# Kernel tuning notes

Measured on AMD Instinct MI355X. Metric: run time of the kernel, lower is better.

The kernel has to match this reference:

```python
import math
import jax, jax.numpy as jnp
import numpy as np

B, S, HID, NH = 8, 512, 1024, 16
D = HID // NH          # head dim = 64
SPAN = 512             # att_span = max_relative_positions = max_position_embeddings


def _linear(x, W, b):
    # torch nn.Linear: y = x @ W.T + b, W is [out, in]
    return jnp.einsum('...i,oi->...o', x, W) + b


def _heads(x):
    # [B, S, HID] -> [B, NH, S, D]
    b, s, _ = x.shape
    return x.reshape(b, s, NH, D).transpose(0, 2, 1, 3)


def setup_inputs() -> dict:
    key = jax.random.key(0)
    ks = jax.random.split(key, 16)
    f = lambda i, shape, sc=1.0: jax.random.normal(ks[i], shape, dtype=jnp.float32) * sc
    return {
        'q': f(0, (B, S, HID)),
        'k': f(1, (B, S, HID)),
        'v': f(2, (B, S, HID)),
        'attention_mask': jnp.tril(jnp.ones((S, S), dtype=bool))[None, None],  # causal [1,1,S,S]
        'Wq': f(3, (HID, HID), 0.02), 'bq': jnp.zeros((HID,), jnp.float32),
        'Wk': f(4, (HID, HID), 0.02), 'bk': jnp.zeros((HID,), jnp.float32),
        'Wv': f(5, (HID, HID), 0.02), 'bv': jnp.zeros((HID,), jnp.float32),
        'Wpk': f(6, (HID, HID), 0.02), 'bpk': jnp.zeros((HID,), jnp.float32),
        'Wpq': f(7, (HID, HID), 0.02), 'bpq': jnp.zeros((HID,), jnp.float32),
        'rel_emb': f(8, (2 * SPAN, HID), 0.02),
    }


def reference(q, k, v, attention_mask, Wq, bq, Wk, bk, Wv, bv, Wpk, bpk, Wpq, bpq, rel_emb):
    scale_factor = 3  # 1 (content) + c2p + p2c
    scale = 1.0 / math.sqrt(D * scale_factor)

    ql = _heads(_linear(q, Wq, bq))   # [B,NH,S,D]
    kl = _heads(_linear(k, Wk, bk))
    vl = _heads(_linear(v, Wv, bv))

    # content-to-content scores
    scores = jnp.einsum('bhqd,bhkd->bhqk', ql, kl) * scale

    # relative positions (no bucketing since position_buckets = -1)
    rel = jnp.arange(S)[:, None] - jnp.arange(S)[None, :]          # [S,S]
    c2p_pos = jnp.clip(rel + SPAN, 0, 2 * SPAN - 1)
    p2c_pos = jnp.clip(-rel + SPAN, 0, 2 * SPAN - 1)

    # projected relative-position embeddings -> [NH, 2*SPAN, D]
    pk = _linear(rel_emb, Wpk, bpk).reshape(2 * SPAN, NH, D).transpose(1, 0, 2)
    pq = _linear(rel_emb, Wpq, bpq).reshape(2 * SPAN, NH, D).transpose(1, 0, 2)

    # content-to-position: out[b,h,q,k] = (q . pos_key)[b,h,q, c2p_pos[q,k]]
    c2p = jnp.einsum('bhqd,hjd->bhqj', ql, pk) * scale             # [B,NH,S,2*SPAN]
    c2p = jnp.take_along_axis(c2p, jnp.broadcast_to(c2p_pos[None, None], (B, NH, S, S)), axis=-1)

    # position-to-content: gathered[b,h,k,q] = (k . pos_query)[b,h,k, p2c_pos[k,q]], then transpose
    p2c = jnp.einsum('bhkd,hjd->bhkj', kl, pq) * scale             # [B,NH,S,2*SPAN]
    p2c = jnp.take_along_axis(p2c, jnp.broadcast_to(p2c_pos[None, None], (B, NH, S, S)), axis=-1)

    scores = scores + c2p + jnp.swapaxes(p2c, -1, -2)
    # subtract detached row max (as in torch: .max(...).values.detach())
    scores = scores - jax.lax.stop_gradient(scores.max(axis=-1, keepdims=True))

    # XSoftmax: masked softmax, then zero masked positions
    neg = jnp.float32(-1e30)
    probs = jax.nn.softmax(jnp.where(attention_mask, scores, neg), axis=-1)
    probs = jnp.where(attention_mask, probs, 0.0)

    ctx = jnp.einsum('bhqk,bhkd->bhqd', probs, vl)                 # [B,NH,S,D]
    return ctx.transpose(0, 2, 1, 3).reshape(B, S, HID)
```

## Files before the change

kernel.cpp:

```cpp
#include <hip/hip_runtime.h>
#include <hip/hip_bf16.h>
#include <math.h>

#define SCALE 0.07216878364870323f
#define NEG_BIG -1e30f

typedef __attribute__((ext_vector_type(8))) short bf16x8;
typedef __attribute__((ext_vector_type(4))) short bf16x4;
typedef __attribute__((ext_vector_type(4))) float f32x4;
#define MFMA_BF16 __builtin_amdgcn_mfma_f32_16x16x32_bf16

static __device__ __forceinline__ float bf2f(__hip_bfloat16 x) { return __bfloat162float(x); }
static __device__ __forceinline__ __hip_bfloat16 f2bf(float x) { return __float2bfloat16(x); }
static __device__ __forceinline__ short f2bs(float x) {
  union { __hip_bfloat16 b; short s; } u; u.b = __float2bfloat16(x); return u.s;
}
static __device__ __forceinline__ float s2f(short v) {
  union { float f; unsigned u; } x; x.u = ((unsigned)(unsigned short)v) << 16; return x.f;
}
static __device__ __forceinline__ bf16x4 cvt4(float4 f) {
  bf16x4 r; r[0] = f2bs(f.x); r[1] = f2bs(f.y); r[2] = f2bs(f.z); r[3] = f2bs(f.w);
  return r;
}
static __device__ __forceinline__ bf16x8 ldg8(const __hip_bfloat16* p) {
  return *(const bf16x8*)p;
}
static __device__ __forceinline__ void gl_lds16(const __hip_bfloat16* g, __hip_bfloat16* l) {
  __builtin_amdgcn_global_load_lds(
      (const __attribute__((address_space(1))) void*)g,
      (__attribute__((address_space(3))) void*)l, 16, 0, 0);
}

struct CvtJob { const float* src; __hip_bfloat16* dst; int n4; };
struct CvtArgs { CvtJob j[9]; };

__global__ __launch_bounds__(256) void cvt_kernel(CvtArgs a) {
  const CvtJob jb = a.j[blockIdx.y];
  const float4* s = (const float4*)jb.src;
  bf16x4* d = (bf16x4*)jb.dst;
  const int stride = gridDim.x * 256;
  for (int i = blockIdx.x * 256 + threadIdx.x; i < jb.n4; i += stride)
    d[i] = cvt4(s[i]);
}

struct Gemm { const __hip_bfloat16* A; const __hip_bfloat16* W;
              const float* bias; __hip_bfloat16* out; int mode; int mBits; int nBlk; };
struct ProjArgs { Gemm g[5]; };

static __device__ __forceinline__ void stage256(const __hip_bfloat16* gbase,
                                                __hip_bfloat16* lbase,
                                                int wave, int lane) {
  const int r = wave * 8 + (lane >> 3);
  const int chunk = (lane & 7) ^ (lane >> 3);
#pragma unroll
  for (int c = 0; c < 4; c++) {
    gl_lds16(gbase + (size_t)(c * 64 + r) * 1024 + chunk * 8,
             lbase + (size_t)(c * 64 + wave * 8) * 64);
  }
}

__global__ __launch_bounds__(512, 2) void proj_kernel(ProjArgs pa) {
  const Gemm g = pa.g[blockIdx.y];
  if ((int)blockIdx.x >= g.nBlk) return;
  __shared__ __hip_bfloat16 As[2][256][64];
  __shared__ __hip_bfloat16 Ws[2][256][64];

  const int bid = blockIdx.x;
  const int m0 = (bid & ((1 << g.mBits) - 1)) * 256;
  const int n0 = (bid >> g.mBits) * 256;
  const int tid = threadIdx.x;
  const int wave = tid >> 6, lane = tid & 63;
  const int q16 = lane >> 4, l16 = lane & 15;
  const int wr = wave >> 2, wc = wave & 3;

  const __hip_bfloat16* Ag = g.A + (size_t)m0 * 1024;
  const __hip_bfloat16* Wg = g.W + (size_t)n0 * 1024;

  f32x4 acc[8][4] = {};

  stage256(Ag, &As[0][0][0], wave, lane);
  stage256(Wg, &Ws[0][0][0], wave, lane);

  const int l7 = l16 & 7;

  for (int t = 0; t < 16; ++t) {
    const int cur = t & 1;
    __syncthreads();
    if (t + 1 < 16) {
      const int k0n = (t + 1) * 64;
      stage256(Ag + k0n, &As[cur ^ 1][0][0], wave, lane);
      stage256(Wg + k0n, &Ws[cur ^ 1][0][0], wave, lane);
    }
    const __hip_bfloat16* Ac = &As[cur][0][0];
    const __hip_bfloat16* Wc = &Ws[cur][0][0];
#pragma unroll
    for (int ki = 0; ki < 2; ki++) {
      const int csw = ((ki * 4 + q16) ^ l7) * 8;
      bf16x8 af[8];
#pragma unroll
      for (int mi = 0; mi < 8; mi++)
        af[mi] = *(const bf16x8*)(Ac + (size_t)(wr * 128 + mi * 16 + l16) * 64 + csw);
#pragma unroll
      for (int ni = 0; ni < 4; ni++) {
        bf16x8 bw = *(const bf16x8*)(Wc + (size_t)(wc * 64 + ni * 16 + l16) * 64 + csw);
#pragma unroll
        for (int mi = 0; mi < 8; mi++)
          acc[mi][ni] = MFMA_BF16(af[mi], bw, acc[mi][ni], 0, 0, 0);
      }
    }
  }

#pragma unroll
  for (int ni = 0; ni < 4; ni++) {
    const int n = n0 + wc * 64 + ni * 16 + l16;
    const int h = n >> 6, d = n & 63;
    const float bv = g.bias[n];
#pragma unroll
    for (int mi = 0; mi < 8; mi++) {
      const int mbase = m0 + wr * 128 + mi * 16 + q16 * 4;
#pragma unroll
      for (int rr = 0; rr < 4; rr++) {
        const int m = mbase + rr;
        const float val = acc[mi][ni][rr] + bv;
        size_t oidx;
        if (g.mode == 0) {
          const int b = m >> 9, s = m & 511;
          oidx = ((size_t)((b * 16 + h) * 512 + s)) * 64 + d;
        } else if (g.mode == 1) {
          const int b = m >> 9, s = m & 511;
          oidx = ((size_t)((b * 16 + h) * 64 + d)) * 512 + s;
        } else {
          oidx = ((size_t)(h * 512 + m)) * 64 + d;
        }
        g.out[oidx] = f2bf(val);
      }
    }
  }
}

__global__ __launch_bounds__(256) void attn_kernel(
    const __hip_bfloat16* __restrict__ ql,
    const __hip_bfloat16* __restrict__ kl,
    const __hip_bfloat16* __restrict__ vlT,
    const __hip_bfloat16* __restrict__ pk,
    const __hip_bfloat16* __restrict__ pq,
    float* __restrict__ out)
{
  __shared__ float rowsum[32];
  __shared__ __align__(16) __hip_bfloat16 sc[32][520];
  __shared__ __align__(16) __hip_bfloat16 ks_[32][72];
  __shared__ __align__(16) __hip_bfloat16 pks[32][72];
  __shared__ __align__(16) __hip_bfloat16 pqs[2][32][72];
  __shared__ __hip_bfloat16 cpb[2][32][34];
  __shared__ __align__(16) __hip_bfloat16 pqbT[2][2][32][36];

  const int bid = blockIdx.x;
  const int qt = 15 - (bid >> 7);
  const int bh = bid & 127;
  const int h = bh & 15, b = bh >> 4;
  const int q0 = qt * 32;

  const __hip_bfloat16* qlp = ql + (size_t)bh * 512 * 64;
  const __hip_bfloat16* klp = kl + (size_t)bh * 512 * 64;
  const __hip_bfloat16* vtp = vlT + (size_t)bh * 64 * 512;
  const __hip_bfloat16* pkp = pk + (size_t)h * 512 * 64;
  const __hip_bfloat16* pqp = pq + (size_t)h * 512 * 64;

  const int tid = threadIdx.x, wave = tid >> 6, lane = tid & 63;
  const int q16 = lane >> 4, l16 = lane & 15;
  const int wr = wave & 1, wc = wave >> 1;

  const int rowQ = q0 + wr * 16 + l16;
  bf16x8 aq0 = ldg8(qlp + (size_t)rowQ * 64 + q16 * 8);
  bf16x8 aq1 = ldg8(qlp + (size_t)rowQ * 64 + 32 + q16 * 8);

  {
    int4 z = {0, 0, 0, 0};
    *(int4*)(&pqs[1][tid >> 3][(tid & 7) * 8]) = z;
  }

  const int kEnd = q0 + 32;
  const int nIter = kEnd >> 5;

  const int sr = tid >> 3, sseg = tid & 7;
  int4 rKv, rPKv, rPQv;
  {
    rKv  = ((const int4*)(klp + (size_t)(q0 + sr) * 64))[sseg];
    rPKv = ((const int4*)(pkp + (size_t)(0 + sr) * 64))[sseg];
    rPQv = ((const int4*)(pqp + (size_t)(0 + sr) * 64))[sseg];
  }

  f32x4 qkPrev = {};
  int k0Prev = 0, parPrev = 0;

  for (int it = 0; it < nIter; ++it) {
    const int k0 = q0 - it * 32;
    const int par = it & 1;
    __syncthreads();
    *(int4*)(&ks_[sr][sseg * 8]) = rKv;
    *(int4*)(&pks[sr][sseg * 8]) = rPKv;
    *(int4*)(&pqs[par][sr][sseg * 8]) = rPQv;
    if (it > 0) {
#pragma unroll
      for (int rr = 0; rr < 4; rr++) {
        const int qh = wr * 16 + q16 * 4 + rr;
        const int kh = wc * 16 + l16;
        if (k0Prev + kh > q0 + qh) {
          sc[qh][k0Prev + kh] = f2bf(NEG_BIG);
        } else {
          const int dlt = qh - kh;
          const float c2pv = (dlt >= 0) ? bf2f(cpb[parPrev][qh][dlt])
                                        : bf2f(cpb[parPrev ^ 1][qh][dlt + 32]);
          const float p2cv = (dlt >= 0) ? bf2f(pqbT[parPrev][1][dlt][kh])
                                        : bf2f(pqbT[parPrev][0][dlt + 32][kh]);
          float v = (qkPrev[rr] + c2pv + p2cv) * SCALE;
          v = fminf(v, 60.f); v = fmaxf(v, -60.f);
          sc[qh][k0Prev + kh] = f2bf(v);
        }
      }
    }
    __syncthreads();
    if (it + 1 < nIter) {
      const int k0n = k0 - 32, jbn = q0 - k0n;
      rKv  = ((const int4*)(klp + (size_t)(k0n + sr) * 64))[sseg];
      rPKv = ((const int4*)(pkp + (size_t)(jbn + sr) * 64))[sseg];
      rPQv = ((const int4*)(pqp + (size_t)(jbn + sr) * 64))[sseg];
    }

    const int rA = wr * 16 + l16;
    const int rB = wc * 16 + l16;
    f32x4 qk = {}, cp = {}, p0 = {}, p1 = {};
#pragma unroll
    for (int ksi = 0; ksi < 2; ksi++) {
      const int ko = ksi * 32 + q16 * 8;
      bf16x8 aq = ksi ? aq1 : aq0;
      bf16x8 ak = *(const bf16x8*)(&ks_[rA][ko]);
      bf16x8 bk = *(const bf16x8*)(&ks_[rB][ko]);
      bf16x8 bp = *(const bf16x8*)(&pks[rB][ko]);
      bf16x8 b1 = *(const bf16x8*)(&pqs[par][rB][ko]);
      bf16x8 b0 = *(const bf16x8*)(&pqs[par ^ 1][rB][ko]);
      qk = MFMA_BF16(aq, bk, qk, 0, 0, 0);
      cp = MFMA_BF16(aq, bp, cp, 0, 0, 0);
      p0 = MFMA_BF16(ak, b0, p0, 0, 0, 0);
      p1 = MFMA_BF16(ak, b1, p1, 0, 0, 0);
    }
    {
      const int cw = wc * 16 + l16;
      const int rwb = wr * 16 + q16 * 4;
      bf16x4 v0, v1;
#pragma unroll
      for (int rr = 0; rr < 4; rr++) {
        cpb[par][rwb + rr][cw] = f2bf(cp[rr]);
        v0[rr] = f2bs(p0[rr]);
        v1[rr] = f2bs(p1[rr]);
      }
      *(bf16x4*)(&pqbT[par][0][cw][rwb]) = v0;
      *(bf16x4*)(&pqbT[par][1][cw][rwb]) = v1;
    }
    qkPrev = qk; k0Prev = k0; parPrev = par;
  }
  __syncthreads();
  {
#pragma unroll
    for (int rr = 0; rr < 4; rr++) {
      const int qh = wr * 16 + q16 * 4 + rr;
      const int kh = wc * 16 + l16;
      if (k0Prev + kh > q0 + qh) {
        sc[qh][k0Prev + kh] = f2bf(NEG_BIG);
      } else {
        const int dlt = qh - kh;
        const float c2pv = (dlt >= 0) ? bf2f(cpb[parPrev][qh][dlt])
                                      : bf2f(cpb[parPrev ^ 1][qh][dlt + 32]);
        const float p2cv = (dlt >= 0) ? bf2f(pqbT[parPrev][1][dlt][kh])
                                      : bf2f(pqbT[parPrev][0][dlt + 32][kh]);
        float v = (qkPrev[rr] + c2pv + p2cv) * SCALE;
        v = fminf(v, 60.f); v = fmaxf(v, -60.f);
        sc[qh][k0Prev + kh] = f2bf(v);
      }
    }
  }
  __syncthreads();

  {
    const int row = tid >> 3, sub = tid & 7;
    float m = NEG_BIG;
    for (int c = sub * 8; c < kEnd; c += 64) {
      bf16x8 x8 = *(const bf16x8*)(&sc[row][c]);
#pragma unroll
      for (int e = 0; e < 8; e++) m = fmaxf(m, s2f(x8[e]));
    }
    for (int off = 1; off < 8; off <<= 1) m = fmaxf(m, __shfl_xor(m, off));
    float s = 0.f;
    for (int c = sub * 8; c < kEnd; c += 64) {
      bf16x8 x8 = *(const bf16x8*)(&sc[row][c]);
      bf16x8 p8;
#pragma unroll
      for (int e = 0; e < 8; e++) {
        const float p = __expf(s2f(x8[e]) - m);
        p8[e] = f2bs(p);
        s += p;
      }
      *(bf16x8*)(&sc[row][c]) = p8;
    }
    for (int off = 1; off < 8; off <<= 1) s += __shfl_xor(s, off);
    if (sub == 0) rowsum[row] = s;
  }

  f32x4 octx[2] = {};
  __hip_bfloat16 (*vt)[72] = (__hip_bfloat16 (*)[72])(&pqs[0][0][0]);
  for (int k0 = 0; k0 < kEnd; k0 += 64) {
    __syncthreads();
    {
      const int r = tid >> 2, seg = tid & 3;
      const int4* src = (const int4*)(vtp + (size_t)r * 512 + k0);
      *(int4*)(&vt[r][seg * 8])       = src[seg];
      *(int4*)(&vt[r][(seg + 4) * 8]) = src[seg + 4];
    }
    __syncthreads();
#pragma unroll
    for (int sub = 0; sub < 2; sub++) {
      const int kk = k0 + sub * 32;
      if (kk < kEnd) {
        bf16x8 af = *(const bf16x8*)(&sc[wr * 16 + l16][kk + q16 * 8]);
#pragma unroll
        for (int cs = 0; cs < 2; cs++) {
          bf16x8 bv = *(const bf16x8*)(&vt[wc * 32 + cs * 16 + l16][sub * 32 + q16 * 8]);
          octx[cs] = MFMA_BF16(af, bv, octx[cs], 0, 0, 0);
        }
      }
    }
  }

  for (int cs = 0; cs < 2; cs++) {
    const int d = wc * 32 + cs * 16 + l16;
    for (int rr = 0; rr < 4; rr++) {
      const int qh = wr * 16 + q16 * 4 + rr;
      const float val = octx[cs][rr] / rowsum[qh];
      out[((size_t)(b * 512 + q0 + qh)) * 1024 + h * 64 + d] = val;
    }
  }
}

extern "C" void kernel_launch(void* const* d_in, const int* in_sizes, int n_in,
                              void* d_out, int out_size, void* d_ws, size_t ws_size,
                              hipStream_t stream) {
  const float* q   = (const float*)d_in[0];
  const float* k   = (const float*)d_in[1];
  const float* v   = (const float*)d_in[2];
  const float* Wq  = (const float*)d_in[4];
  const float* bq  = (const float*)d_in[5];
  const float* Wk  = (const float*)d_in[6];
  const float* bk  = (const float*)d_in[7];
  const float* Wv  = (const float*)d_in[8];
  const float* bv  = (const float*)d_in[9];
  const float* Wpk = (const float*)d_in[10];
  const float* bpk = (const float*)d_in[11];
  const float* Wpq = (const float*)d_in[12];
  const float* bpq = (const float*)d_in[13];
  const float* rel = (const float*)d_in[14];
  float* out = (float*)d_out;

  char* ws = (char*)d_ws;
  const size_t MB = 1u << 20;
  __hip_bfloat16* bqi  = (__hip_bfloat16*)(ws);
  __hip_bfloat16* bki  = (__hip_bfloat16*)(ws + 8 * MB);
  __hip_bfloat16* bvi  = (__hip_bfloat16*)(ws + 16 * MB);
  __hip_bfloat16* bWq  = (__hip_bfloat16*)(ws + 24 * MB);
  __hip_bfloat16* bWk  = (__hip_bfloat16*)(ws + 26 * MB);
  __hip_bfloat16* bWv  = (__hip_bfloat16*)(ws + 28 * MB);
  __hip_bfloat16* bWpk = (__hip_bfloat16*)(ws + 30 * MB);
  __hip_bfloat16* bWpq = (__hip_bfloat16*)(ws + 32 * MB);
  __hip_bfloat16* brel = (__hip_bfloat16*)(ws + 34 * MB);
  __hip_bfloat16* wql  = (__hip_bfloat16*)(ws + 35 * MB);
  __hip_bfloat16* wkl  = (__hip_bfloat16*)(ws + 43 * MB);
  __hip_bfloat16* wvlT = (__hip_bfloat16*)(ws + 51 * MB);
  __hip_bfloat16* wpk  = (__hip_bfloat16*)(ws + 59 * MB);
  __hip_bfloat16* wpq  = (__hip_bfloat16*)(ws + 60 * MB);

  CvtArgs ca;
  ca.j[0] = { q,   bqi,  4194304 / 4 };
  ca.j[1] = { k,   bki,  4194304 / 4 };
  ca.j[2] = { v,   bvi,  4194304 / 4 };
  ca.j[3] = { Wq,  bWq,  1048576 / 4 };
  ca.j[4] = { Wk,  bWk,  1048576 / 4 };
  ca.j[5] = { Wv,  bWv,  1048576 / 4 };
  ca.j[6] = { Wpk, bWpk, 1048576 / 4 };
  ca.j[7] = { Wpq, bWpq, 1048576 / 4 };
  ca.j[8] = { rel + (size_t)512 * 1024, brel, 524288 / 4 };
  cvt_kernel<<<dim3(1024, 9), 256, 0, stream>>>(ca);

  ProjArgs pj;
  pj.g[0] = { bqi,  bWq,  bq,  wql,  0, 4, 64 };
  pj.g[1] = { bki,  bWk,  bk,  wkl,  0, 4, 64 };
  pj.g[2] = { bvi,  bWv,  bv,  wvlT, 1, 4, 64 };
  pj.g[3] = { brel, bWpk, bpk, wpk,  2, 1, 8 };
  pj.g[4] = { brel, bWpq, bpq, wpq,  2, 1, 8 };
  proj_kernel<<<dim3(64, 5), 512, 0, stream>>>(pj);

  attn_kernel<<<2048, 256, 0, stream>>>(wql, wkl, wvlT, wpk, wpq, out);
}
```

Baseline: 248.8 us.

## Interleave half-tile prefetch with MFMA phases and swap V projection operands

The projection GEMM main loop now issues its global-to-LDS prefetch in half-tile pieces spread across the four MFMA phases. It replaces __syncthreads with explicit s_barrier and vmcnt waits and raises wave priority around the MFMA bursts, so loads overlap with math instead of being issued in one block. The V projection is also computed as W·X^T (operands swapped) so the transposed output is written with contiguous stores along the sequence dimension. The hand-managed waitcnt/barrier sequencing is fragile and could race if the counts are wrong.

```diff
diff --git a/kernel.cpp b/kernel.cpp
--- a/kernel.cpp
+++ b/kernel.cpp
@@ -9,6 +9,10 @@
 typedef __attribute__((ext_vector_type(4))) short bf16x4;
 typedef __attribute__((ext_vector_type(4))) float f32x4;
 #define MFMA_BF16 __builtin_amdgcn_mfma_f32_16x16x32_bf16
+
+#define BARX()   asm volatile("s_barrier" ::: "memory")
+#define VMCNT2() asm volatile("s_waitcnt vmcnt(2)" ::: "memory")
+#define VMCNT0() asm volatile("s_waitcnt vmcnt(0)" ::: "memory")
 
 static __device__ __forceinline__ float bf2f(__hip_bfloat16 x) { return __bfloat162float(x); }
 static __device__ __forceinline__ __hip_bfloat16 f2bf(float x) { return __float2bfloat16(x); }
@@ -47,15 +51,16 @@
               const float* bias; __hip_bfloat16* out; int mode; int mBits; int nBlk; };
 struct ProjArgs { Gemm g[5]; };
 
-static __device__ __forceinline__ void stage256(const __hip_bfloat16* gbase,
-                                                __hip_bfloat16* lbase,
-                                                int wave, int lane) {
-  const int r = wave * 8 + (lane >> 3);
-  const int chunk = (lane & 7) ^ (lane >> 3);
-#pragma unroll
-  for (int c = 0; c < 4; c++) {
-    gl_lds16(gbase + (size_t)(c * 64 + r) * 1024 + chunk * 8,
-             lbase + (size_t)(c * 64 + wave * 8) * 64);
+static __device__ __forceinline__ void stage_half(const __hip_bfloat16* gtile,
+                                                  __hip_bfloat16* ltile,
+                                                  int half, int wave, int lane) {
+  const int r = lane >> 3;
+  const int chunk = (lane & 7) ^ r;
+#pragma unroll
+  for (int c = 0; c < 2; c++) {
+    const int rowbase = half * 128 + c * 64 + wave * 8;
+    gl_lds16(gtile + (size_t)(rowbase + r) * 1024 + chunk * 8,
+             ltile + (size_t)rowbase * 64);
   }
 }
 
@@ -72,64 +77,93 @@
   const int wave = tid >> 6, lane = tid & 63;
   const int q16 = lane >> 4, l16 = lane & 15;
   const int wr = wave >> 2, wc = wave & 3;
+  const int l7 = l16 & 7;
 
   const __hip_bfloat16* Ag = g.A + (size_t)m0 * 1024;
   const __hip_bfloat16* Wg = g.W + (size_t)n0 * 1024;
 
   f32x4 acc[8][4] = {};
 
-  stage256(Ag, &As[0][0][0], wave, lane);
-  stage256(Wg, &Ws[0][0][0], wave, lane);
-
-  const int l7 = l16 & 7;
+  stage_half(Ag, &As[0][0][0], 0, wave, lane);
+  stage_half(Ag, &As[0][0][0], 1, wave, lane);
+  stage_half(Wg, &Ws[0][0][0], 0, wave, lane);
+  stage_half(Wg, &Ws[0][0][0], 1, wave, lane);
+  stage_half(Ag + 64, &As[1][0][0], 0, wave, lane);
+  VMCNT2();
+  BARX();
 
   for (int t = 0; t < 16; ++t) {
     const int cur = t & 1;
-    __syncthreads();
-    if (t + 1 < 16) {
-      const int k0n = (t + 1) * 64;
-      stage256(Ag + k0n, &As[cur ^ 1][0][0], wave, lane);
-      stage256(Wg + k0n, &Ws[cur ^ 1][0][0], wave, lane);
-    }
     const __hip_bfloat16* Ac = &As[cur][0][0];
     const __hip_bfloat16* Wc = &Ws[cur][0][0];
-#pragma unroll
-    for (int ki = 0; ki < 2; ki++) {
-      const int csw = ((ki * 4 + q16) ^ l7) * 8;
-      bf16x8 af[8];
-#pragma unroll
-      for (int mi = 0; mi < 8; mi++)
-        af[mi] = *(const bf16x8*)(Ac + (size_t)(wr * 128 + mi * 16 + l16) * 64 + csw);
-#pragma unroll
-      for (int ni = 0; ni < 4; ni++) {
-        bf16x8 bw = *(const bf16x8*)(Wc + (size_t)(wc * 64 + ni * 16 + l16) * 64 + csw);
-#pragma unroll
-        for (int mi = 0; mi < 8; mi++)
-          acc[mi][ni] = MFMA_BF16(af[mi], bw, acc[mi][ni], 0, 0, 0);
-      }
-    }
+    __hip_bfloat16* An = &As[cur ^ 1][0][0];
+    __hip_bfloat16* Wn = &Ws[cur ^ 1][0][0];
+    const __hip_bfloat16* gAn = Ag + (size_t)(t + 1) * 64;
+    const __hip_bfloat16* gWn = Wg + (size_t)(t + 1) * 64;
+    const bool pf = (t + 1 < 16);
+
+#pragma unroll
+    for (int kh = 0; kh < 2; kh++) {
+      const int csw = ((kh * 4 + q16) ^ l7) * 8;
+      bf16x8 bw[4];
+#pragma unroll
+      for (int ni = 0; ni < 4; ni++)
+        bw[ni] = *(const bf16x8*)(Wc + (size_t)(wc * 64 + ni * 16 + l16) * 64 + csw);
+#pragma unroll
+      for (int mh = 0; mh < 2; mh++) {
+        bf16x8 af[4];
+#pragma unroll
+        for (int mi = 0; mi < 4; mi++)
+          af[mi] = *(const bf16x8*)(Ac + (size_t)(wr * 128 + mh * 64 + mi * 16 + l16) * 64 + csw);
+        const int ph = kh * 2 + mh;
+        if (pf) {
+          if (ph == 0)      stage_half(gAn, An, 1, wave, lane);
+          else if (ph == 1) stage_half(gWn, Wn, 0, wave, lane);
+          else if (ph == 2) stage_half(gWn, Wn, 1, wave, lane);
+        }
+        __builtin_amdgcn_s_setprio(1);
+#pragma unroll
+        for (int ni = 0; ni < 4; ni++)
+#pragma unroll
+          for (int mi = 0; mi < 4; mi++)
+            acc[mh * 4 + mi][ni] =
+                MFMA_BF16(af[mi], bw[ni], acc[mh * 4 + mi][ni], 0, 0, 0);
+        __builtin_amdgcn_s_setprio(0);
+      }
+    }
+    BARX();
+    if (t + 2 < 16) {
+      stage_half(Ag + (size_t)(t + 2) * 64, &As[cur][0][0], 0, wave, lane);
+      VMCNT2();
+    } else {
+      VMCNT0();
+    }
+    BARX();
   }
 
 #pragma unroll
   for (int ni = 0; ni < 4; ni++) {
     const int n = n0 + wc * 64 + ni * 16 + l16;
-    const int h = n >> 6, d = n & 63;
-    const float bv = g.bias[n];
 #pragma unroll
     for (int mi = 0; mi < 8; mi++) {
-      const int mbase = m0 + wr * 128 + mi * 16 + q16 * 4;
 #pragma unroll
       for (int rr = 0; rr < 4; rr++) {
-        const int m = mbase + rr;
-        const float val = acc[mi][ni][rr] + bv;
+        const int m = m0 + wr * 128 + mi * 16 + q16 * 4 + rr;
+        float val = acc[mi][ni][rr];
         size_t oidx;
         if (g.mode == 0) {
+          val += g.bias[n];
           const int b = m >> 9, s = m & 511;
+          const int h = n >> 6, d = n & 63;
           oidx = ((size_t)((b * 16 + h) * 512 + s)) * 64 + d;
         } else if (g.mode == 1) {
-          const int b = m >> 9, s = m & 511;
+          val += g.bias[m];
+          const int b = n >> 9, s = n & 511;
+          const int h = m >> 6, d = m & 63;
           oidx = ((size_t)((b * 16 + h) * 64 + d)) * 512 + s;
         } else {
+          val += g.bias[n];
+          const int h = n >> 6, d = n & 63;
           oidx = ((size_t)(h * 512 + m)) * 64 + d;
         }
         g.out[oidx] = f2bf(val);
@@ -392,7 +426,7 @@
   ProjArgs pj;
   pj.g[0] = { bqi,  bWq,  bq,  wql,  0, 4, 64 };
   pj.g[1] = { bki,  bWk,  bk,  wkl,  0, 4, 64 };
-  pj.g[2] = { bvi,  bWv,  bv,  wvlT, 1, 4, 64 };
+  pj.g[2] = { bWv,  bvi,  bv,  wvlT, 1, 2, 64 };
   pj.g[3] = { brel, bWpk, bpk, wpk,  2, 1, 8 };
   pj.g[4] = { brel, bWpq, bpq, wpq,  2, 1, 8 };
   proj_kernel<<<dim3(64, 5), 512, 0, stream>>>(pj);
```

Result: faster. 242.0 us (-2.7%).
